# Performance work log

Hardware: AMD Instinct MI355X
Metric: run time of the kernel (lower is better)

The kernel has to match this reference:

```python
import jax, jax.numpy as jnp
import numpy as np

N = 100000      # nodes
E = 1600000     # edges
IN = 128        # in_channels
HID = 32        # hidden_channels
HEADS = 4
G = 256         # number of graphs in the batch
NEG_SLOPE = 0.2


def setup_inputs() -> dict:
    key = jax.random.key(0)
    ks = jax.random.split(key, 20)
    s = 0.1
    d = {
        'x': jax.random.normal(ks[0], (N, IN), jnp.float32),
        'edge_index': jax.random.randint(ks[1], (2, E), 0, N, dtype=jnp.int64),
        'batch': jnp.sort(jax.random.randint(ks[2], (N,), 0, G, dtype=jnp.int64)),
        # conv1: IN -> HID per head, HEADS heads, concat
        'W1': jax.random.normal(ks[3], (IN, HEADS * HID), jnp.float32) * s,
        'a_src1': jax.random.normal(ks[4], (HEADS, HID), jnp.float32) * s,
        'a_dst1': jax.random.normal(ks[5], (HEADS, HID), jnp.float32) * s,
        'b1': jnp.zeros((HEADS * HID,), jnp.float32),
        # conv2: HEADS*HID -> HID per head, HEADS heads, concat
        'W2': jax.random.normal(ks[6], (HEADS * HID, HEADS * HID), jnp.float32) * s,
        'a_src2': jax.random.normal(ks[7], (HEADS, HID), jnp.float32) * s,
        'a_dst2': jax.random.normal(ks[8], (HEADS, HID), jnp.float32) * s,
        'b2': jnp.zeros((HEADS * HID,), jnp.float32),
        # conv3: HEADS*HID -> HID, 1 head, no concat (mean over heads is identity)
        'W3': jax.random.normal(ks[9], (HEADS * HID, HID), jnp.float32) * s,
        'a_src3': jax.random.normal(ks[10], (1, HID), jnp.float32) * s,
        'a_dst3': jax.random.normal(ks[11], (1, HID), jnp.float32) * s,
        'b3': jnp.zeros((HID,), jnp.float32),
        # final readout
        'fc_w': jax.random.normal(ks[12], (HID, 1), jnp.float32) * s,
        'fc_b': jnp.zeros((1,), jnp.float32),
    }
    return d


def _gat_layer(x, src, dst, W, a_s, a_d, b, concat):
    """One PyG-style GATConv: edge attention logits, per-destination softmax, scatter-aggregate."""
    n = x.shape[0]
    H, C = a_s.shape
    h = (x @ W).reshape(n, H, C)                       # [N, H, C]
    asrc = (h * a_s).sum(-1)                           # [N, H]
    adst = (h * a_d).sum(-1)                           # [N, H]
    e = jax.nn.leaky_relu(asrc[src] + adst[dst], NEG_SLOPE)   # [Etot, H]
    m = jax.ops.segment_max(e, dst, num_segments=n)    # per-dst max (self-loops guarantee non-empty)
    ex = jnp.exp(e - m[dst])
    den = jax.ops.segment_sum(ex, dst, num_segments=n)
    alpha = ex / (den[dst] + 1e-16)                    # segment softmax, [Etot, H]
    out = jax.ops.segment_sum(alpha[:, :, None] * h[src], dst, num_segments=n)  # [N, H, C]
    if concat:
        return out.reshape(n, H * C) + b
    return out.mean(axis=1) + b


def reference(x, edge_index, batch, W1, a_src1, a_dst1, b1, W2, a_src2, a_dst2, b2,
              W3, a_src3, a_dst3, b3, fc_w, fc_b):
    n = x.shape[0]
    loops = jnp.arange(n, dtype=edge_index.dtype)      # GATConv adds self-loops by default
    src = jnp.concatenate([edge_index[0], loops])
    dst = jnp.concatenate([edge_index[1], loops])

    h = jax.nn.elu(_gat_layer(x, src, dst, W1, a_src1, a_dst1, b1, True))
    h = jax.nn.elu(_gat_layer(h, src, dst, W2, a_src2, a_dst2, b2, True))
    h = jax.nn.elu(_gat_layer(h, src, dst, W3, a_src3, a_dst3, b3, False))

    counts = jax.ops.segment_sum(jnp.ones((n,), h.dtype), batch, num_segments=G)
    pooled = jax.ops.segment_sum(h, batch, num_segments=G) / jnp.maximum(counts, 1.0)[:, None]
    # dropout p=0.5 is identity in eval mode
    return pooled @ fc_w + fc_b                        # [G, 1]
```

## Files before the change

kernel.cpp:

```cpp
#include <hip/hip_runtime.h>
#include <hip/hip_bf16.h>
#include <math.h>

#define NEG_SLOPE 0.2f
#define CHUNK 6144

typedef short bf16x8 __attribute__((ext_vector_type(8)));
typedef float f32x4  __attribute__((ext_vector_type(4)));

__device__ __forceinline__ float leaky(float x){ return x > 0.f ? x : NEG_SLOPE*x; }
__device__ __forceinline__ float elu(float x){ return x > 0.f ? x : expm1f(x); }

__device__ __forceinline__ ushort f2bf(float f){
  uint u = __float_as_uint(f);
  u += 0x7fffu + ((u >> 16) & 1u);
  return (ushort)(u >> 16);
}
__device__ __forceinline__ uint pk2(float lo, float hi){
  return (uint)f2bf(lo) | ((uint)f2bf(hi) << 16);
}
__device__ __forceinline__ float2 bfpair(uint v){
  return make_float2(__uint_as_float(v << 16), __uint_as_float(v & 0xffff0000u));
}

__global__ __launch_bounds__(256) void k_histA(const int* __restrict__ ei, int E,
                                               int* __restrict__ bucketCount){
  __shared__ int hist[512];
  for (int b = threadIdx.x; b < 512; b += 256) hist[b] = 0;
  __syncthreads();
  int base = blockIdx.x * 2048;
  int cnt = min(2048, E - base);
  for (int i = threadIdx.x; i < cnt; i += 256)
    atomicAdd(&hist[ei[E + base + i] >> 8], 1);
  __syncthreads();
  for (int b = threadIdx.x; b < 512; b += 256)
    if (hist[b]) atomicAdd(&bucketCount[b], hist[b]);
}

__global__ __launch_bounds__(256) void k_scanB(const int* __restrict__ bucketCount, int NB,
                        int* __restrict__ bucketBase, int* __restrict__ gcursor, int E){
  __shared__ int s[512];
  for (int b = threadIdx.x; b < 512; b += 256)
    s[b] = (b < NB) ? bucketCount[b] : 0;
  __syncthreads();
  if (threadIdx.x == 0){
    int run = 0;
    for (int b = 0; b < NB; b++){ int v = s[b]; s[b] = run; run += v; }
  }
  __syncthreads();
  for (int b = threadIdx.x; b < NB; b += 256){
    bucketBase[b] = s[b]; gcursor[b] = s[b];
  }
  if (threadIdx.x == 0) bucketBase[NB] = E;
}

__global__ __launch_bounds__(256) void k_scatA(const int* __restrict__ ei, int E, int NB,
                         int* __restrict__ gcursor, uint* __restrict__ tmp){
  __shared__ uint stageS[CHUNK];
  __shared__ uint stageD[CHUNK];
  __shared__ int hist[512], pre[512], cur[512], gbase[512];
  __shared__ int scanArr[256];
  int tid = threadIdx.x;
  int base = blockIdx.x * CHUNK;
  int cnt = min(CHUNK, E - base);
  for (int b = tid; b < 512; b += 256) hist[b] = 0;
  __syncthreads();
  for (int i = tid; i < cnt; i += 256)
    atomicAdd(&hist[ei[E + base + i] >> 8], 1);
  __syncthreads();
  int a0 = hist[2*tid], a1 = hist[2*tid+1];
  scanArr[tid] = a0 + a1;
  __syncthreads();
  for (int st = 1; st < 256; st <<= 1){
    int v = (tid >= st) ? scanArr[tid - st] : 0;
    __syncthreads();
    scanArr[tid] += v;
    __syncthreads();
  }
  int eb = tid ? scanArr[tid-1] : 0;
  pre[2*tid] = eb;        cur[2*tid] = eb;
  pre[2*tid+1] = eb + a0; cur[2*tid+1] = eb + a0;
  if (2*tid < NB && a0 > 0)   gbase[2*tid]   = atomicAdd(&gcursor[2*tid],   a0);
  if (2*tid+1 < NB && a1 > 0) gbase[2*tid+1] = atomicAdd(&gcursor[2*tid+1], a1);
  __syncthreads();
  for (int i = tid; i < cnt; i += 256){
    int s = ei[base + i];
    int d = ei[E + base + i];
    int lpos = atomicAdd(&cur[d >> 8], 1);
    stageS[lpos] = (uint)s; stageD[lpos] = (uint)d;
  }
  __syncthreads();
  for (int i = tid; i < cnt; i += 256){
    uint d = stageD[i];
    int b = d >> 8;
    tmp[gbase[b] + (i - pre[b])] = (stageS[i] << 8) | (d & 255u);
  }
}

__global__ __launch_bounds__(256) void k_csr(const uint* __restrict__ tmp,
                      const int* __restrict__ bucketBase,
                      int N, int NB, int* __restrict__ offsets, int* __restrict__ csr){
  int b = blockIdx.x;
  int nodeBase = b << 8;
  int nNodes = min(256, N - nodeBase);
  int eBeg = bucketBase[b], eEnd = bucketBase[b+1];
  __shared__ int deg[256], cur[256];
  int tid = threadIdx.x;
  deg[tid] = 0;
  __syncthreads();
  for (int e = eBeg + tid; e < eEnd; e += 256)
    atomicAdd(&deg[tmp[e] & 255u], 1);
  __syncthreads();
  cur[tid] = deg[tid];
  __syncthreads();
  for (int st = 1; st < 256; st <<= 1){
    int w = (tid >= st) ? cur[tid - st] : 0;
    __syncthreads();
    cur[tid] += w;
    __syncthreads();
  }
  int excl = tid ? cur[tid-1] : 0;
  __syncthreads();
  cur[tid] = excl;
  if (tid < nNodes) offsets[nodeBase + tid] = eBeg + excl;
  if (b == NB-1 && tid == 0) offsets[N] = eEnd;
  __syncthreads();
  for (int e = eBeg + tid; e < eEnd; e += 256){
    uint u = tmp[e];
    int lpos = atomicAdd(&cur[u & 255u], 1);
    csr[eBeg + lpos] = (int)(u >> 8);
  }
}

template<int NT, int H>
__device__ __forceinline__ void wrep_dev(const float* __restrict__ W,
                    const float* __restrict__ a_s, const float* __restrict__ a_d,
                    ushort* __restrict__ Wf, int idx){
  constexpr int NTT = NT + 1;
  constexpr int M = NT*16;
  if (idx >= NTT*4*64) return;
  int lane = idx & 63;
  int c = (idx >> 6) & 3;
  int t = idx >> 8;
  int j = lane & 15;
  int k0 = c*32 + (lane >> 4)*8;
  float vals[8];
  if (t < NT){
    int col = t*16 + j;
    const float* p0 = W + (size_t)k0*M + col;
    #pragma unroll
    for (int r = 0; r < 8; r++) vals[r] = p0[(size_t)r*M];
  } else {
    #pragma unroll
    for (int r = 0; r < 8; r++) vals[r] = 0.f;
    if (j < 2*H){
      int h = (j < H) ? j : (j - H);
      const float* av = (j < H) ? (a_s + h*32) : (a_d + h*32);
      #pragma unroll
      for (int r = 0; r < 8; r++){
        const float* wr = W + (size_t)(k0 + r)*M + h*32;
        float s = 0.f;
        for (int cc = 0; cc < 32; cc++) s += wr[cc]*av[cc];
        vals[r] = s;
      }
    }
  }
  uint4 o;
  o.x = pk2(vals[0], vals[1]); o.y = pk2(vals[2], vals[3]);
  o.z = pk2(vals[4], vals[5]); o.w = pk2(vals[6], vals[7]);
  *(uint4*)(Wf + (size_t)idx*8) = o;
}

__global__ __launch_bounds__(256) void k_wrepAll(
    const float* __restrict__ W1, const float* __restrict__ as1, const float* __restrict__ ad1, ushort* __restrict__ Wf1,
    const float* __restrict__ W2, const float* __restrict__ as2, const float* __restrict__ ad2, ushort* __restrict__ Wf2,
    const float* __restrict__ W3, const float* __restrict__ as3, const float* __restrict__ ad3, ushort* __restrict__ Wf3){
  int b = blockIdx.x;
  if (b < 9)       wrep_dev<8,4>(W1, as1, ad1, Wf1, b*256 + threadIdx.x);
  else if (b < 18) wrep_dev<8,4>(W2, as2, ad2, Wf2, (b-9)*256 + threadIdx.x);
  else             wrep_dev<2,1>(W3, as3, ad3, Wf3, (b-18)*256 + threadIdx.x);
}

template<int NT, bool A_F32, int H>
__global__ __launch_bounds__(256) void k_mgemm(const void* __restrict__ Xv,
                     const ushort* __restrict__ Wf, ushort* __restrict__ Y,
                     float* __restrict__ asrc, float* __restrict__ adst, int n){
  constexpr int NTT = NT + 1;
  constexpr int M = NT*16;
  int lane = threadIdx.x & 63;
  int l15 = lane & 15, q = lane >> 4;
  int wgid = blockIdx.x*4 + (threadIdx.x >> 6);
  int nchunks = (n + 15) >> 4;
  int stride = gridDim.x*4;

  bf16x8 bw[NTT][4];
  #pragma unroll
  for (int t = 0; t < NTT; t++)
    #pragma unroll
    for (int c = 0; c < 4; c++)
      bw[t][c] = *(const bf16x8*)(Wf + (size_t)(((t<<2)+c)*64 + lane)*8);

  int chunk = wgid;
  if (chunk >= nchunks) return;

  bf16x8 aCur[4], aNext[4];
  auto loadA = [&](int ck, bf16x8* a){
    int m = ck*16 + l15;
    if (m >= n) m = n - 1;
    if (A_F32){
      const float* X = (const float*)Xv + (size_t)m*128 + q*8;
      #pragma unroll
      for (int c = 0; c < 4; c++){
        float4 u0 = *(const float4*)(X + c*32);
        float4 u1 = *(const float4*)(X + c*32 + 4);
        uint4 pkd;
        pkd.x = pk2(u0.x, u0.y); pkd.y = pk2(u0.z, u0.w);
        pkd.z = pk2(u1.x, u1.y); pkd.w = pk2(u1.z, u1.w);
        union { uint4 u; bf16x8 v; } cv; cv.u = pkd;
        a[c] = cv.v;
      }
    } else {
      const ushort* X = (const ushort*)Xv + (size_t)m*128 + q*8;
      #pragma unroll
      for (int c = 0; c < 4; c++) a[c] = *(const bf16x8*)(X + c*32);
    }
  };

  loadA(chunk, aCur);
  while (true){
    int nx = chunk + stride;
    if (nx < nchunks) loadA(nx, aNext);
    f32x4 acc[NTT];
    #pragma unroll
    for (int t = 0; t < NTT; t++) acc[t] = (f32x4){0.f,0.f,0.f,0.f};
    #pragma unroll
    for (int c = 0; c < 4; c++)
      #pragma unroll
      for (int t = 0; t < NTT; t++)
        acc[t] = __builtin_amdgcn_mfma_f32_16x16x32_bf16(aCur[c], bw[t][c], acc[t], 0, 0, 0);
    int rowb = chunk*16 + q*4;
    #pragma unroll
    for (int t = 0; t < NT; t++)
      #pragma unroll
      for (int r = 0; r < 4; r++){
        int row = rowb + r;
        if (row < n) Y[(size_t)row*M + t*16 + l15] = f2bf(acc[t][r]);
      }
    #pragma unroll
    for (int r = 0; r < 4; r++){
      int row = rowb + r;
      if (row < n){
        float v = acc[NT][r];
        if (l15 < H)           asrc[(size_t)row*H + l15]       = v;
        else if (l15 < 2*H)    adst[(size_t)row*H + (l15 - H)] = v;
      }
    }
    if (nx >= nchunks) break;
    chunk = nx;
    #pragma unroll
    for (int c = 0; c < 4; c++) aCur[c] = aNext[c];
  }
}

template<bool OUT_BF16>
__global__ __launch_bounds__(256) void k_agg128f(const ushort* __restrict__ Hb,
                    const float* __restrict__ asrc, const float* __restrict__ adst,
                    const int* __restrict__ offsets, const int* __restrict__ csr_src,
                    const float* __restrict__ bias, void* __restrict__ Out, int n){
  __shared__ float lwAll[4][256];
  int wv = threadIdx.x >> 6;
  int lane = threadIdx.x & 63;
  float* lw = lwAll[wv];
  int node = blockIdx.x*4 + wv;
  if (node >= n) return;
  const int up = lane, ch = up*2, h0 = up >> 4;
  const uint* rows = (const uint*)Hb;
  int j0 = offsets[node], end = offsets[node+1];
  float4 adv = *(const float4*)(adst + (size_t)node*4);
  float adh = (h0==0)?adv.x:(h0==1)?adv.y:(h0==2)?adv.z:adv.w;
  float acc0 = 0.f, acc1 = 0.f, den = 0.f;
  {
    float w = __expf(leaky(asrc[(size_t)node*4 + h0] + adh));
    float2 f = bfpair(rows[(size_t)node*64 + up]);
    den += w; acc0 += w*f.x; acc1 += w*f.y;
  }
  for (int base = j0; base < end; base += 64){
    int m = min(64, end - base);
    int mR = (m + 7) & ~7;
    int sreg = node;
    if (lane < m){
      sreg = csr_src[base + lane];
      float4 a = *(const float4*)(asrc + (size_t)sreg*4);
      float4 w4;
      w4.x = __expf(leaky(a.x + adv.x));
      w4.y = __expf(leaky(a.y + adv.y));
      w4.z = __expf(leaky(a.z + adv.z));
      w4.w = __expf(leaky(a.w + adv.w));
      *(float4*)(lw + lane*4) = w4;
    } else if (lane < mR){
      *(float4*)(lw + lane*4) = make_float4(0.f, 0.f, 0.f, 0.f);
    }
    uint rA[8]; float wA[8];
    uint rB[8]; float wB[8];
    auto loadGroup = [&](int e, uint* r, float* w){
      #pragma unroll
      for (int k = 0; k < 8; k++){
        int s = __builtin_amdgcn_readlane(sreg, e + k);
        r[k] = rows[(size_t)(uint)s*64 + up];
      }
      #pragma unroll
      for (int k = 0; k < 8; k++) w[k] = lw[(e + k)*4 + h0];
    };
    auto consume = [&](const uint* r, const float* w){
      #pragma unroll
      for (int k = 0; k < 8; k++){
        float2 f = bfpair(r[k]);
        den += w[k]; acc0 += w[k]*f.x; acc1 += w[k]*f.y;
      }
    };
    loadGroup(0, rA, wA);
    int e = 8;
    for (; e + 16 <= mR; e += 16){
      loadGroup(e, rB, wB);
      consume(rA, wA);
      loadGroup(e + 8, rA, wA);
      consume(rB, wB);
    }
    if (e < mR){
      loadGroup(e, rB, wB);
      consume(rA, wA);
      consume(rB, wB);
    } else {
      consume(rA, wA);
    }
  }
  float inv = 1.f/(den + 1e-16f);
  float ox = elu(acc0*inv + bias[ch]);
  float oy = elu(acc1*inv + bias[ch+1]);
  if (OUT_BF16){
    ((uint*)Out)[(size_t)node*64 + up] = pk2(ox, oy);
  } else {
    *(float2*)((float*)Out + (size_t)node*128 + ch) = make_float2(ox, oy);
  }
}

__global__ __launch_bounds__(256) void k_agg32pool(const ushort* __restrict__ Hb,
                    const float* __restrict__ asrc, const float* __restrict__ adst,
                    const int* __restrict__ offsets, const int* __restrict__ csr_src,
                    const float* __restrict__ bias, const float* __restrict__ fcw,
                    const int* __restrict__ batch, float* __restrict__ pool, int n){
  __shared__ int   lsAll[4][4][16];
  __shared__ float lwAll[4][4][16];
  int wv = threadIdx.x >> 6;
  int lane = threadIdx.x & 63;
  int g = lane >> 4, i = lane & 15;
  int node = (blockIdx.x*4 + wv)*4 + g;
  if (node >= n) return;
  int* ls = lsAll[wv][g];
  float* lw = lwAll[wv][g];
  const uint* rows = (const uint*)Hb;
  float adn = adst[node];
  float acc0 = 0.f, acc1 = 0.f, den = 0.f;
  {
    float w = __expf(leaky(asrc[node] + adn));
    float2 f = bfpair(rows[(size_t)node*16 + i]);
    den += w; acc0 += w*f.x; acc1 += w*f.y;
  }
  int j0 = offsets[node], end = offsets[node+1];
  for (int base = j0; base < end; base += 16){
    int m = min(16, end - base);
    {
      int idx = base + i;
      bool v = idx < end;
      int s = v ? csr_src[idx] : node;
      ls[i] = s;
      lw[i] = v ? __expf(leaky(asrc[s] + adn)) : 0.f;
    }
    int mR = (m + 3) & ~3;
    for (int e = 0; e < mR; e += 4){
      int s0 = ls[e], s1 = ls[e+1], s2 = ls[e+2], s3 = ls[e+3];
      float w0 = lw[e], w1 = lw[e+1], w2 = lw[e+2], w3 = lw[e+3];
      uint r0 = rows[(size_t)s0*16 + i];
      uint r1 = rows[(size_t)s1*16 + i];
      uint r2 = rows[(size_t)s2*16 + i];
      uint r3 = rows[(size_t)s3*16 + i];
      float2 f0 = bfpair(r0), f1 = bfpair(r1), f2 = bfpair(r2), f3 = bfpair(r3);
      den  += (w0 + w1) + (w2 + w3);
      acc0 += w0*f0.x + w1*f1.x + w2*f2.x + w3*f3.x;
      acc1 += w0*f0.y + w1*f1.y + w2*f2.y + w3*f3.y;
    }
  }
  float inv = 1.f/(den + 1e-16f);
  int ch = i*2;
  float2 fw = *(const float2*)(fcw + ch);
  float t = elu(acc0*inv + bias[ch])*fw.x + elu(acc1*inv + bias[ch+1])*fw.y;
  #pragma unroll
  for (int off = 1; off < 16; off <<= 1) t += __shfl_xor(t, off, 16);
  if (i == 0) atomicAdd(&pool[(size_t)batch[node]*16 + (node & 15)], t);
}

__global__ __launch_bounds__(256) void k_bounds(const int* __restrict__ batch, int n, int G,
                                                int* __restrict__ gstart){
  int i = blockIdx.x*256 + threadIdx.x;
  if (i >= n) return;
  int b = batch[i];
  int bp = (i > 0) ? batch[i-1] : -1;
  for (int g = bp + 1; g <= b; g++) gstart[g] = i;
  if (i == n-1){
    for (int g = b + 1; g <= G; g++) gstart[g] = n;
  }
}

__global__ __launch_bounds__(256) void k_poolfin(const float* __restrict__ pool,
                    const int* __restrict__ gstart, const float* __restrict__ fcb,
                    float* __restrict__ out, int G){
  int g = blockIdx.x*256 + threadIdx.x;
  if (g >= G) return;
  float s = 0.f;
  #pragma unroll
  for (int k = 0; k < 16; k++) s += pool[(size_t)g*16 + k];
  float cnt = (float)(gstart[g+1] - gstart[g]);
  if (cnt < 1.f) cnt = 1.f;
  out[g] = s/cnt + fcb[0];
}

extern "C" void kernel_launch(void* const* d_in, const int* in_sizes, int n_in,
                              void* d_out, int out_size, void* d_ws, size_t ws_size,
                              hipStream_t stream){
  const float* x    = (const float*)d_in[0];
  const int*   ei   = (const int*)d_in[1];
  const int*   batch= (const int*)d_in[2];
  const float* W1   = (const float*)d_in[3];
  const float* as1  = (const float*)d_in[4];
  const float* ad1  = (const float*)d_in[5];
  const float* b1   = (const float*)d_in[6];
  const float* W2   = (const float*)d_in[7];
  const float* as2  = (const float*)d_in[8];
  const float* ad2  = (const float*)d_in[9];
  const float* b2   = (const float*)d_in[10];
  const float* W3   = (const float*)d_in[11];
  const float* as3  = (const float*)d_in[12];
  const float* ad3  = (const float*)d_in[13];
  const float* b3   = (const float*)d_in[14];
  const float* fcw  = (const float*)d_in[15];
  const float* fcb  = (const float*)d_in[16];
  float* out = (float*)d_out;

  const int N = in_sizes[0] / 128;
  const int E = in_sizes[1] / 2;
  const int G = out_size;
  const int NB = (N + 255) >> 8;

  char* p = (char*)d_ws;
  auto alloc = [&](size_t bytes) -> void* {
    void* r = (void*)p;
    p += (bytes + 255) & ~(size_t)255;
    return r;
  };
  ushort* bufH   = (ushort*)alloc((size_t)N*128*sizeof(ushort));
  ushort* aggB   = (ushort*)alloc((size_t)N*128*sizeof(ushort));
  ushort* bufH3  = (ushort*)alloc((size_t)N*32*sizeof(ushort));
  float*  asrcA  = (float*)alloc((size_t)N*4*sizeof(float));
  float*  adstA  = (float*)alloc((size_t)N*4*sizeof(float));
  float*  asrcB  = (float*)alloc((size_t)N*4*sizeof(float));
  float*  adstB  = (float*)alloc((size_t)N*4*sizeof(float));
  int*    offsets= (int*)alloc((size_t)(N+1)*sizeof(int));
  int*    csr    = (int*)alloc((size_t)E*sizeof(int));
  uint*   tmp    = (uint*)alloc((size_t)E*sizeof(uint));
  int*    bCount = (int*)alloc(512*sizeof(int));
  int*    bBase  = (int*)alloc(520*sizeof(int));
  int*    gcursor= (int*)alloc(512*sizeof(int));
  int*    gstart = (int*)alloc((size_t)(G+1)*sizeof(int));
  float*  pool   = (float*)alloc((size_t)G*16*sizeof(float));
  ushort* Wf1    = (ushort*)alloc(9*4*64*8*sizeof(ushort));
  ushort* Wf2    = (ushort*)alloc(9*4*64*8*sizeof(ushort));
  ushort* Wf3    = (ushort*)alloc(3*4*64*8*sizeof(ushort));

  hipMemsetAsync(bCount, 0, 512*sizeof(int), stream);
  hipMemsetAsync(pool, 0, (size_t)G*16*sizeof(float), stream);

  k_wrepAll<<<21, 256, 0, stream>>>(W1, as1, ad1, Wf1, W2, as2, ad2, Wf2, W3, as3, ad3, Wf3);

  k_histA<<<(E+2047)/2048, 256, 0, stream>>>(ei, E, bCount);
  k_scanB<<<1, 256, 0, stream>>>(bCount, NB, bBase, gcursor, E);
  k_scatA<<<(E+CHUNK-1)/CHUNK, 256, 0, stream>>>(ei, E, NB, gcursor, tmp);
  k_csr<<<NB, 256, 0, stream>>>(tmp, bBase, N, NB, offsets, csr);
  k_bounds<<<(N+255)/256, 256, 0, stream>>>(batch, N, G, gstart);

  const int GB = (((N + 15)/16) + 3)/4;
  const int NWB = (N + 3)/4;
  const int NWB32 = (N + 15)/16;
  k_mgemm<8, true , 4><<<GB, 256, 0, stream>>>(x, Wf1, bufH, asrcA, adstA, N);
  k_agg128f<true><<<NWB, 256, 0, stream>>>(bufH, asrcA, adstA, offsets, csr, b1, aggB, N);
  k_mgemm<8, false, 4><<<GB, 256, 0, stream>>>(aggB, Wf2, bufH, asrcB, adstB, N);
  k_agg128f<true><<<NWB, 256, 0, stream>>>(bufH, asrcB, adstB, offsets, csr, b2, aggB, N);
  k_mgemm<2, false, 1><<<GB, 256, 0, stream>>>(aggB, Wf3, bufH3, asrcA, adstA, N);
  k_agg32pool<<<NWB32, 256, 0, stream>>>(bufH3, asrcA, adstA, offsets, csr,
                                         b3, fcw, batch, pool, N);
  k_poolfin<<<(G+255)/256, 256, 0, stream>>>(pool, gstart, fcb, out, G);
}
```

Before: 433.6 us.

## Fuse preprocessing kernels and fold pool finalize into last aggregation block

Merges weight repacking, pool zeroing, graph-boundary computation and the bucket histogram into a single prep kernel. The separate scan kernel is removed: scatter and CSR kernels now recompute bucket prefix sums locally from the counts. The pool finalize kernel becomes a last-block-done epilogue in the final aggregation kernel, driven by an atomic counter. This cuts several launches and a memset, at the cost of redundant per-block scans and a threadfence per node group.

```diff
diff --git a/kernel.cpp b/kernel.cpp
--- a/kernel.cpp
+++ b/kernel.cpp
@@ -21,115 +21,6 @@
 }
 __device__ __forceinline__ float2 bfpair(uint v){
   return make_float2(__uint_as_float(v << 16), __uint_as_float(v & 0xffff0000u));
-}
-
-__global__ __launch_bounds__(256) void k_histA(const int* __restrict__ ei, int E,
-                                               int* __restrict__ bucketCount){
-  __shared__ int hist[512];
-  for (int b = threadIdx.x; b < 512; b += 256) hist[b] = 0;
-  __syncthreads();
-  int base = blockIdx.x * 2048;
-  int cnt = min(2048, E - base);
-  for (int i = threadIdx.x; i < cnt; i += 256)
-    atomicAdd(&hist[ei[E + base + i] >> 8], 1);
-  __syncthreads();
-  for (int b = threadIdx.x; b < 512; b += 256)
-    if (hist[b]) atomicAdd(&bucketCount[b], hist[b]);
-}
-
-__global__ __launch_bounds__(256) void k_scanB(const int* __restrict__ bucketCount, int NB,
-                        int* __restrict__ bucketBase, int* __restrict__ gcursor, int E){
-  __shared__ int s[512];
-  for (int b = threadIdx.x; b < 512; b += 256)
-    s[b] = (b < NB) ? bucketCount[b] : 0;
-  __syncthreads();
-  if (threadIdx.x == 0){
-    int run = 0;
-    for (int b = 0; b < NB; b++){ int v = s[b]; s[b] = run; run += v; }
-  }
-  __syncthreads();
-  for (int b = threadIdx.x; b < NB; b += 256){
-    bucketBase[b] = s[b]; gcursor[b] = s[b];
-  }
-  if (threadIdx.x == 0) bucketBase[NB] = E;
-}
-
-__global__ __launch_bounds__(256) void k_scatA(const int* __restrict__ ei, int E, int NB,
-                         int* __restrict__ gcursor, uint* __restrict__ tmp){
-  __shared__ uint stageS[CHUNK];
-  __shared__ uint stageD[CHUNK];
-  __shared__ int hist[512], pre[512], cur[512], gbase[512];
-  __shared__ int scanArr[256];
-  int tid = threadIdx.x;
-  int base = blockIdx.x * CHUNK;
-  int cnt = min(CHUNK, E - base);
-  for (int b = tid; b < 512; b += 256) hist[b] = 0;
-  __syncthreads();
-  for (int i = tid; i < cnt; i += 256)
-    atomicAdd(&hist[ei[E + base + i] >> 8], 1);
-  __syncthreads();
-  int a0 = hist[2*tid], a1 = hist[2*tid+1];
-  scanArr[tid] = a0 + a1;
-  __syncthreads();
-  for (int st = 1; st < 256; st <<= 1){
-    int v = (tid >= st) ? scanArr[tid - st] : 0;
-    __syncthreads();
-    scanArr[tid] += v;
-    __syncthreads();
-  }
-  int eb = tid ? scanArr[tid-1] : 0;
-  pre[2*tid] = eb;        cur[2*tid] = eb;
-  pre[2*tid+1] = eb + a0; cur[2*tid+1] = eb + a0;
-  if (2*tid < NB && a0 > 0)   gbase[2*tid]   = atomicAdd(&gcursor[2*tid],   a0);
-  if (2*tid+1 < NB && a1 > 0) gbase[2*tid+1] = atomicAdd(&gcursor[2*tid+1], a1);
-  __syncthreads();
-  for (int i = tid; i < cnt; i += 256){
-    int s = ei[base + i];
-    int d = ei[E + base + i];
-    int lpos = atomicAdd(&cur[d >> 8], 1);
-    stageS[lpos] = (uint)s; stageD[lpos] = (uint)d;
-  }
-  __syncthreads();
-  for (int i = tid; i < cnt; i += 256){
-    uint d = stageD[i];
-    int b = d >> 8;
-    tmp[gbase[b] + (i - pre[b])] = (stageS[i] << 8) | (d & 255u);
-  }
-}
-
-__global__ __launch_bounds__(256) void k_csr(const uint* __restrict__ tmp,
-                      const int* __restrict__ bucketBase,
-                      int N, int NB, int* __restrict__ offsets, int* __restrict__ csr){
-  int b = blockIdx.x;
-  int nodeBase = b << 8;
-  int nNodes = min(256, N - nodeBase);
-  int eBeg = bucketBase[b], eEnd = bucketBase[b+1];
-  __shared__ int deg[256], cur[256];
-  int tid = threadIdx.x;
-  deg[tid] = 0;
-  __syncthreads();
-  for (int e = eBeg + tid; e < eEnd; e += 256)
-    atomicAdd(&deg[tmp[e] & 255u], 1);
-  __syncthreads();
-  cur[tid] = deg[tid];
-  __syncthreads();
-  for (int st = 1; st < 256; st <<= 1){
-    int w = (tid >= st) ? cur[tid - st] : 0;
-    __syncthreads();
-    cur[tid] += w;
-    __syncthreads();
-  }
-  int excl = tid ? cur[tid-1] : 0;
-  __syncthreads();
-  cur[tid] = excl;
-  if (tid < nNodes) offsets[nodeBase + tid] = eBeg + excl;
-  if (b == NB-1 && tid == 0) offsets[N] = eEnd;
-  __syncthreads();
-  for (int e = eBeg + tid; e < eEnd; e += 256){
-    uint u = tmp[e];
-    int lpos = atomicAdd(&cur[u & 255u], 1);
-    csr[eBeg + lpos] = (int)(u >> 8);
-  }
 }
 
 template<int NT, int H>
@@ -171,14 +62,148 @@
   *(uint4*)(Wf + (size_t)idx*8) = o;
 }
 
-__global__ __launch_bounds__(256) void k_wrepAll(
+__global__ __launch_bounds__(256) void k_prep(
     const float* __restrict__ W1, const float* __restrict__ as1, const float* __restrict__ ad1, ushort* __restrict__ Wf1,
     const float* __restrict__ W2, const float* __restrict__ as2, const float* __restrict__ ad2, ushort* __restrict__ Wf2,
-    const float* __restrict__ W3, const float* __restrict__ as3, const float* __restrict__ ad3, ushort* __restrict__ Wf3){
+    const float* __restrict__ W3, const float* __restrict__ as3, const float* __restrict__ ad3, ushort* __restrict__ Wf3,
+    const int* __restrict__ ei, int E, int* __restrict__ bucketCount,
+    const int* __restrict__ batch, int N, int G, int* __restrict__ gstart,
+    float* __restrict__ pool, int* __restrict__ done, int NBb){
+  __shared__ int hist[512];
   int b = blockIdx.x;
-  if (b < 9)       wrep_dev<8,4>(W1, as1, ad1, Wf1, b*256 + threadIdx.x);
-  else if (b < 18) wrep_dev<8,4>(W2, as2, ad2, Wf2, (b-9)*256 + threadIdx.x);
-  else             wrep_dev<2,1>(W3, as3, ad3, Wf3, (b-18)*256 + threadIdx.x);
+  int tid = threadIdx.x;
+  if (b < 9){ wrep_dev<8,4>(W1, as1, ad1, Wf1, b*256 + tid); return; }
+  if (b < 18){ wrep_dev<8,4>(W2, as2, ad2, Wf2, (b-9)*256 + tid); return; }
+  if (b < 21){ wrep_dev<2,1>(W3, as3, ad3, Wf3, (b-18)*256 + tid); return; }
+  if (b == 21){
+    for (int i = tid; i < G*16; i += 256) pool[i] = 0.f;
+    if (tid == 0) *done = 0;
+    return;
+  }
+  b -= 22;
+  if (b < NBb){
+    int i = b*256 + tid;
+    if (i >= N) return;
+    int bb = batch[i];
+    int bp = (i > 0) ? batch[i-1] : -1;
+    for (int g = bp + 1; g <= bb; g++) gstart[g] = i;
+    if (i == N-1){
+      for (int g = bb + 1; g <= G; g++) gstart[g] = N;
+    }
+    return;
+  }
+  b -= NBb;
+  for (int k = tid; k < 512; k += 256) hist[k] = 0;
+  __syncthreads();
+  int base = b * 2048;
+  int cnt = min(2048, E - base);
+  for (int i = tid; i < cnt; i += 256)
+    atomicAdd(&hist[ei[E + base + i] >> 8], 1);
+  __syncthreads();
+  for (int k = tid; k < 512; k += 256)
+    if (hist[k]) atomicAdd(&bucketCount[k], hist[k]);
+}
+
+__global__ __launch_bounds__(256) void k_scatA(const int* __restrict__ ei, int E, int NB,
+                         const int* __restrict__ bucketCount,
+                         int* __restrict__ gcursor, uint* __restrict__ tmp){
+  __shared__ uint stageS[CHUNK];
+  __shared__ uint stageD[CHUNK];
+  __shared__ int hist[512], pre[512], cur[512], gbase[512], bbase[512];
+  __shared__ int scanArr[256];
+  int tid = threadIdx.x;
+  int base = blockIdx.x * CHUNK;
+  int cnt = min(CHUNK, E - base);
+  int c0 = (2*tid < NB) ? bucketCount[2*tid] : 0;
+  int c1 = (2*tid+1 < NB) ? bucketCount[2*tid+1] : 0;
+  scanArr[tid] = c0 + c1;
+  __syncthreads();
+  for (int st = 1; st < 256; st <<= 1){
+    int v = (tid >= st) ? scanArr[tid - st] : 0;
+    __syncthreads();
+    scanArr[tid] += v;
+    __syncthreads();
+  }
+  int gb = tid ? scanArr[tid-1] : 0;
+  bbase[2*tid] = gb;
+  bbase[2*tid+1] = gb + c0;
+  hist[2*tid] = 0; hist[2*tid+1] = 0;
+  __syncthreads();
+  for (int i = tid; i < cnt; i += 256)
+    atomicAdd(&hist[ei[E + base + i] >> 8], 1);
+  __syncthreads();
+  int a0 = hist[2*tid], a1 = hist[2*tid+1];
+  scanArr[tid] = a0 + a1;
+  __syncthreads();
+  for (int st = 1; st < 256; st <<= 1){
+    int v = (tid >= st) ? scanArr[tid - st] : 0;
+    __syncthreads();
+    scanArr[tid] += v;
+    __syncthreads();
+  }
+  int eb = tid ? scanArr[tid-1] : 0;
+  pre[2*tid] = eb;        cur[2*tid] = eb;
+  pre[2*tid+1] = eb + a0; cur[2*tid+1] = eb + a0;
+  if (2*tid < NB && a0 > 0)   gbase[2*tid]   = bbase[2*tid]   + atomicAdd(&gcursor[2*tid],   a0);
+  if (2*tid+1 < NB && a1 > 0) gbase[2*tid+1] = bbase[2*tid+1] + atomicAdd(&gcursor[2*tid+1], a1);
+  __syncthreads();
+  for (int i = tid; i < cnt; i += 256){
+    int s = ei[base + i];
+    int d = ei[E + base + i];
+    int lpos = atomicAdd(&cur[d >> 8], 1);
+    stageS[lpos] = (uint)s; stageD[lpos] = (uint)d;
+  }
+  __syncthreads();
+  for (int i = tid; i < cnt; i += 256){
+    uint d = stageD[i];
+    int b = d >> 8;
+    tmp[gbase[b] + (i - pre[b])] = (stageS[i] << 8) | (d & 255u);
+  }
+}
+
+__global__ __launch_bounds__(256) void k_csr(const uint* __restrict__ tmp,
+                      const int* __restrict__ bucketCount,
+                      int N, int NB, int* __restrict__ offsets, int* __restrict__ csr){
+  int b = blockIdx.x;
+  int nodeBase = b << 8;
+  int nNodes = min(256, N - nodeBase);
+  int tid = threadIdx.x;
+  __shared__ int red[256];
+  int partial = 0;
+  for (int i = tid; i < b; i += 256) partial += bucketCount[i];
+  red[tid] = partial;
+  __syncthreads();
+  for (int st = 128; st; st >>= 1){
+    if (tid < st) red[tid] += red[tid + st];
+    __syncthreads();
+  }
+  int eBeg = red[0];
+  int eEnd = eBeg + bucketCount[b];
+  __shared__ int deg[256], cur[256];
+  deg[tid] = 0;
+  __syncthreads();
+  for (int e = eBeg + tid; e < eEnd; e += 256)
+    atomicAdd(&deg[tmp[e] & 255u], 1);
+  __syncthreads();
+  cur[tid] = deg[tid];
+  __syncthreads();
+  for (int st = 1; st < 256; st <<= 1){
+    int w = (tid >= st) ? cur[tid - st] : 0;
+    __syncthreads();
+    cur[tid] += w;
+    __syncthreads();
+  }
+  int excl = tid ? cur[tid-1] : 0;
+  __syncthreads();
+  cur[tid] = excl;
+  if (tid < nNodes) offsets[nodeBase + tid] = eBeg + excl;
+  if (b == NB-1 && tid == 0) offsets[N] = eEnd;
+  __syncthreads();
+  for (int e = eBeg + tid; e < eEnd; e += 256){
+    uint u = tmp[e];
+    int lpos = atomicAdd(&cur[u & 255u], 1);
+    csr[eBeg + lpos] = (int)(u >> 8);
+  }
 }
 
 template<int NT, bool A_F32, int H>
@@ -348,80 +373,79 @@
                     const float* __restrict__ asrc, const float* __restrict__ adst,
                     const int* __restrict__ offsets, const int* __restrict__ csr_src,
                     const float* __restrict__ bias, const float* __restrict__ fcw,
-                    const int* __restrict__ batch, float* __restrict__ pool, int n){
+                    const int* __restrict__ batch, float* __restrict__ pool, int n,
+                    const int* __restrict__ gstart, const float* __restrict__ fcb,
+                    float* __restrict__ out, int* __restrict__ done, int G){
   __shared__ int   lsAll[4][4][16];
   __shared__ float lwAll[4][4][16];
+  __shared__ int lastFlag;
   int wv = threadIdx.x >> 6;
   int lane = threadIdx.x & 63;
   int g = lane >> 4, i = lane & 15;
   int node = (blockIdx.x*4 + wv)*4 + g;
-  if (node >= n) return;
-  int* ls = lsAll[wv][g];
-  float* lw = lwAll[wv][g];
-  const uint* rows = (const uint*)Hb;
-  float adn = adst[node];
-  float acc0 = 0.f, acc1 = 0.f, den = 0.f;
-  {
-    float w = __expf(leaky(asrc[node] + adn));
-    float2 f = bfpair(rows[(size_t)node*16 + i]);
-    den += w; acc0 += w*f.x; acc1 += w*f.y;
-  }
-  int j0 = offsets[node], end = offsets[node+1];
-  for (int base = j0; base < end; base += 16){
-    int m = min(16, end - base);
+  if (node < n){
+    int* ls = lsAll[wv][g];
+    float* lw = lwAll[wv][g];
+    const uint* rows = (const uint*)Hb;
+    float adn = adst[node];
+    float acc0 = 0.f, acc1 = 0.f, den = 0.f;
     {
-      int idx = base + i;
-      bool v = idx < end;
-      int s = v ? csr_src[idx] : node;
-      ls[i] = s;
-      lw[i] = v ? __expf(leaky(asrc[s] + adn)) : 0.f;
-    }
-    int mR = (m + 3) & ~3;
-    for (int e = 0; e < mR; e += 4){
-      int s0 = ls[e], s1 = ls[e+1], s2 = ls[e+2], s3 = ls[e+3];
-      float w0 = lw[e], w1 = lw[e+1], w2 = lw[e+2], w3 = lw[e+3];
-      uint r0 = rows[(size_t)s0*16 + i];
-      uint r1 = rows[(size_t)s1*16 + i];
-      uint r2 = rows[(size_t)s2*16 + i];
-      uint r3 = rows[(size_t)s3*16 + i];
-      float2 f0 = bfpair(r0), f1 = bfpair(r1), f2 = bfpair(r2), f3 = bfpair(r3);
-      den  += (w0 + w1) + (w2 + w3);
-      acc0 += w0*f0.x + w1*f1.x + w2*f2.x + w3*f3.x;
-      acc1 += w0*f0.y + w1*f1.y + w2*f2.y + w3*f3.y;
-    }
-  }
-  float inv = 1.f/(den + 1e-16f);
-  int ch = i*2;
-  float2 fw = *(const float2*)(fcw + ch);
-  float t = elu(acc0*inv + bias[ch])*fw.x + elu(acc1*inv + bias[ch+1])*fw.y;
-  #pragma unroll
-  for (int off = 1; off < 16; off <<= 1) t += __shfl_xor(t, off, 16);
-  if (i == 0) atomicAdd(&pool[(size_t)batch[node]*16 + (node & 15)], t);
-}
-
-__global__ __launch_bounds__(256) void k_bounds(const int* __restrict__ batch, int n, int G,
-                                                int* __restrict__ gstart){
-  int i = blockIdx.x*256 + threadIdx.x;
-  if (i >= n) return;
-  int b = batch[i];
-  int bp = (i > 0) ? batch[i-1] : -1;
-  for (int g = bp + 1; g <= b; g++) gstart[g] = i;
-  if (i == n-1){
-    for (int g = b + 1; g <= G; g++) gstart[g] = n;
-  }
-}
-
-__global__ __launch_bounds__(256) void k_poolfin(const float* __restrict__ pool,
-                    const int* __restrict__ gstart, const float* __restrict__ fcb,
-                    float* __restrict__ out, int G){
-  int g = blockIdx.x*256 + threadIdx.x;
-  if (g >= G) return;
-  float s = 0.f;
-  #pragma unroll
-  for (int k = 0; k < 16; k++) s += pool[(size_t)g*16 + k];
-  float cnt = (float)(gstart[g+1] - gstart[g]);
-  if (cnt < 1.f) cnt = 1.f;
-  out[g] = s/cnt + fcb[0];
+      float w = __expf(leaky(asrc[node] + adn));
+      float2 f = bfpair(rows[(size_t)node*16 + i]);
+      den += w; acc0 += w*f.x; acc1 += w*f.y;
+    }
+    int j0 = offsets[node], end = offsets[node+1];
+    for (int base = j0; base < end; base += 16){
+      int m = min(16, end - base);
+      {
+        int idx = base + i;
+        bool v = idx < end;
+        int s = v ? csr_src[idx] : node;
+        ls[i] = s;
+        lw[i] = v ? __expf(leaky(asrc[s] + adn)) : 0.f;
+      }
+      int mR = (m + 3) & ~3;
+      for (int e = 0; e < mR; e += 4){
+        int s0 = ls[e], s1 = ls[e+1], s2 = ls[e+2], s3 = ls[e+3];
+        float w0 = lw[e], w1 = lw[e+1], w2 = lw[e+2], w3 = lw[e+3];
+        uint r0 = rows[(size_t)s0*16 + i];
+        uint r1 = rows[(size_t)s1*16 + i];
+        uint r2 = rows[(size_t)s2*16 + i];
+        uint r3 = rows[(size_t)s3*16 + i];
+        float2 f0 = bfpair(r0), f1 = bfpair(r1), f2 = bfpair(r2), f3 = bfpair(r3);
+        den  += (w0 + w1) + (w2 + w3);
+        acc0 += w0*f0.x + w1*f1.x + w2*f2.x + w3*f3.x;
+        acc1 += w0*f0.y + w1*f1.y + w2*f2.y + w3*f3.y;
+      }
+    }
+    float inv = 1.f/(den + 1e-16f);
+    int ch = i*2;
+    float2 fw = *(const float2*)(fcw + ch);
+    float t = elu(acc0*inv + bias[ch])*fw.x + elu(acc1*inv + bias[ch+1])*fw.y;
+    #pragma unroll
+    for (int off = 1; off < 16; off <<= 1) t += __shfl_xor(t, off, 16);
+    if (i == 0){
+      atomicAdd(&pool[(size_t)batch[node]*16 + (node & 15)], t);
+      __threadfence();
+    }
+  }
+  __syncthreads();
+  if (threadIdx.x == 0){
+    int old = atomicAdd(done, 1);
+    lastFlag = (old == (int)gridDim.x - 1) ? 1 : 0;
+  }
+  __syncthreads();
+  if (lastFlag){
+    for (int gg = threadIdx.x; gg < G; gg += 256){
+      float s = 0.f;
+      #pragma unroll
+      for (int k = 0; k < 16; k++)
+        s += atomicAdd(&pool[(size_t)gg*16 + k], 0.f);
+      float cnt = (float)(gstart[gg+1] - gstart[gg]);
+      if (cnt < 1.f) cnt = 1.f;
+      out[gg] = s/cnt + fcb[0];
+    }
+  }
 }
 
 extern "C" void kernel_launch(void* const* d_in, const int* in_sizes, int n_in,
@@ -467,25 +491,25 @@
   int*    offsets= (int*)alloc((size_t)(N+1)*sizeof(int));
   int*    csr    = (int*)alloc((size_t)E*sizeof(int));
   uint*   tmp    = (uint*)alloc((size_t)E*sizeof(uint));
-  int*    bCount = (int*)alloc(512*sizeof(int));
-  int*    bBase  = (int*)alloc(520*sizeof(int));
-  int*    gcursor= (int*)alloc(512*sizeof(int));
+  int*    zeroR  = (int*)alloc(1024*sizeof(int));
+  int*    bCount = zeroR;
+  int*    gcursor= zeroR + 512;
   int*    gstart = (int*)alloc((size_t)(G+1)*sizeof(int));
   float*  pool   = (float*)alloc((size_t)G*16*sizeof(float));
+  int*    done   = (int*)alloc(256);
   ushort* Wf1    = (ushort*)alloc(9*4*64*8*sizeof(ushort));
   ushort* Wf2    = (ushort*)alloc(9*4*64*8*sizeof(ushort));
   ushort* Wf3    = (ushort*)alloc(3*4*64*8*sizeof(ushort));
 
-  hipMemsetAsync(bCount, 0, 512*sizeof(int), stream);
-  hipMemsetAsync(pool, 0, (size_t)G*16*sizeof(float), stream);
-
-  k_wrepAll<<<21, 256, 0, stream>>>(W1, as1, ad1, Wf1, W2, as2, ad2, Wf2, W3, as3, ad3, Wf3);
-
-  k_histA<<<(E+2047)/2048, 256, 0, stream>>>(ei, E, bCount);
-  k_scanB<<<1, 256, 0, stream>>>(bCount, NB, bBase, gcursor, E);
-  k_scatA<<<(E+CHUNK-1)/CHUNK, 256, 0, stream>>>(ei, E, NB, gcursor, tmp);
-  k_csr<<<NB, 256, 0, stream>>>(tmp, bBase, N, NB, offsets, csr);
-  k_bounds<<<(N+255)/256, 256, 0, stream>>>(batch, N, G, gstart);
+  hipMemsetAsync(zeroR, 0, 1024*sizeof(int), stream);
+
+  const int NBb = (N + 255)/256;
+  const int NH  = (E + 2047)/2048;
+  k_prep<<<22 + NBb + NH, 256, 0, stream>>>(W1, as1, ad1, Wf1, W2, as2, ad2, Wf2,
+                                            W3, as3, ad3, Wf3, ei, E, bCount,
+                                            batch, N, G, gstart, pool, done, NBb);
+  k_scatA<<<(E+CHUNK-1)/CHUNK, 256, 0, stream>>>(ei, E, NB, bCount, gcursor, tmp);
+  k_csr<<<NB, 256, 0, stream>>>(tmp, bCount, N, NB, offsets, csr);
 
   const int GB = (((N + 15)/16) + 3)/4;
   const int NWB = (N + 3)/4;
@@ -496,6 +520,6 @@
   k_agg128f<true><<<NWB, 256, 0, stream>>>(bufH, asrcB, adstB, offsets, csr, b2, aggB, N);
   k_mgemm<2, false, 1><<<GB, 256, 0, stream>>>(aggB, Wf3, bufH3, asrcA, adstA, N);
   k_agg32pool<<<NWB32, 256, 0, stream>>>(bufH3, asrcA, adstA, offsets, csr,
-                                         b3, fcw, batch, pool, N);
-  k_poolfin<<<(G+255)/256, 256, 0, stream>>>(pool, gstart, fcb, out, G);
-}
+                                         b3, fcw, batch, pool, N,
+                                         gstart, fcb, out, done, G);
+}
```

New measurement: 878.9 us. +102.7%, slower.
